# Kernel optimization log

Measured on AMD Instinct MI355X. Metric: run time of the kernel, lower is better.

The kernel has to match this reference:

```python
import jax, jax.numpy as jnp
import numpy as np

EPS = 1e-5


def _bn(x, g, b, axis):
    # training-mode BatchNorm1d (biased variance, eps=1e-5)
    m = x.mean(axis=axis, keepdims=True)
    v = x.var(axis=axis, keepdims=True)
    return (x - m) * jax.lax.rsqrt(v + EPS) * g + b


def _masked_softmax(s, mask):
    # softmax over each node's neighbor set; exact zeros elsewhere
    neg = jnp.finfo(s.dtype).min
    m = jnp.max(jnp.where(mask, s, neg), axis=-1, keepdims=True)
    p = jnp.where(mask, jnp.exp(s - m), 0.0)
    return p / p.sum(axis=-1, keepdims=True)


def _gcn_layer(xh, W, b, g, beta, Wa, ba, mask, apply_act):
    # xh: [H,N,Din] -> [H,N,Dout]; per-head Linear + BatchNorm over nodes
    h = jnp.einsum('hnd,hdo->hno', xh, W) + b[:, None, :]
    h = _bn(h, g[:, None, :], beta[:, None, :], axis=1)
    # dense GAT-style scores [H,N,N], LeakyReLU(0.2)
    s = jnp.einsum('hno,hom->hnm', h, Wa) + ba[:, None, :]
    s = jnp.where(s >= 0, s, 0.2 * s)
    # original detaches scores (numpy roundtrip) -> no grad through attention
    att = jax.lax.stop_gradient(_masked_softmax(s, mask))
    out = jnp.einsum('hnm,hmo->hno', att, h)
    return jax.nn.elu(out) if apply_act else out


def _forward(x, adj_mask, target_X, target,
             W0, b0, g0, beta0, Wa0, ba0,
             W1, b1, g1, beta1, Wa1, ba1,
             bng, bnb, Wp1, bp1, gp1, betap1, Wp2, bp2):
    H = W0.shape[0]
    xh = jnp.broadcast_to(x[None], (H,) + x.shape)            # replicate per head
    h = _gcn_layer(xh, W0, b0, g0, beta0, Wa0, ba0, adj_mask, True)
    h = _gcn_layer(h, W1, b1, g1, beta1, Wa1, ba1, adj_mask, False)
    out = h.sum(axis=0) / H                                    # head average [N,out]
    out = jax.nn.elu(_bn(out, bng, bnb, axis=0))
    y = jax.nn.elu(_bn(out @ Wp1 + bp1, gp1, betap1, axis=0))  # pred1
    y = y @ Wp2 + bp2                                          # pred2
    logits = y[target_X]                                       # [T,C]
    logp = jax.nn.log_softmax(logits, axis=-1)
    loss = -jnp.take_along_axis(logp, target[:, None], axis=-1).mean()
    return loss, logits


def setup_inputs() -> dict:
    key = jax.random.key(0)
    N, H, IN, H1, OUT, PRED, C, T, DEG = 4096, 4, 512, 256, 128, 64, 8, 512, 32
    ks = jax.random.split(key, 16)
    rng = np.random.default_rng(0)
    nbr = rng.integers(0, N, size=(N, DEG))
    mask = np.zeros((N, N), dtype=bool)
    mask[np.arange(N)[:, None], nbr] = True  # every row non-empty

    def lin(k, fan_in, shape):
        return jax.random.normal(k, shape, jnp.float32) / np.sqrt(fan_in)

    return {
        'x': jax.random.normal(ks[0], (N, IN), jnp.float32),
        'adj_mask': jnp.asarray(mask),
        'target_X': jax.random.randint(ks[1], (T,), 0, N),
        'target': jax.random.randint(ks[2], (T,), 0, C),
        'W0': lin(ks[3], IN, (H, IN, H1)), 'b0': jnp.zeros((H, H1)),
        'g0': jnp.ones((H, H1)), 'beta0': jnp.zeros((H, H1)),
        'Wa0': lin(ks[4], H1, (H, H1, N)), 'ba0': jnp.zeros((H, N)),
        'W1': lin(ks[5], H1, (H, H1, OUT)), 'b1': jnp.zeros((H, OUT)),
        'g1': jnp.ones((H, OUT)), 'beta1': jnp.zeros((H, OUT)),
        'Wa1': lin(ks[6], OUT, (H, OUT, N)), 'ba1': jnp.zeros((H, N)),
        'bng': jnp.ones((OUT,)), 'bnb': jnp.zeros((OUT,)),
        'Wp1': lin(ks[7], OUT, (OUT, PRED)), 'bp1': jnp.zeros((PRED,)),
        'gp1': jnp.ones((PRED,)), 'betap1': jnp.zeros((PRED,)),
        'Wp2': lin(ks[8], PRED, (PRED, C)), 'bp2': jnp.zeros((C,)),
    }


def reference(x, adj_mask, target_X, target,
              W0, b0, g0, beta0, Wa0, ba0,
              W1, b1, g1, beta1, Wa1, ba1,
              bng, bnb, Wp1, bp1, gp1, betap1, Wp2, bp2):
    return _forward(x, adj_mask, target_X, target,
                    W0, b0, g0, beta0, Wa0, ba0,
                    W1, b1, g1, beta1, Wa1, ba1,
                    bng, bnb, Wp1, bp1, gp1, betap1, Wp2, bp2)
```

## Files before the change

### kernel.cpp

```cpp
#include <hip/hip_runtime.h>
#include <hip/hip_bf16.h>
#include <math.h>

#define NN   4096
#define HH   4
#define DIN  512
#define DH1  256
#define DOUT 128
#define DPRED 64
#define NCLS 8
#define NT   512
#define NBMAX 32
#define BNCH 128

typedef __attribute__((ext_vector_type(4))) float f32x4;
typedef __attribute__((ext_vector_type(8))) short bf16x8;
typedef __attribute__((ext_vector_type(8))) unsigned short u16x8;

#define SWZ(o) ((o) + (((o) >> 5) << 2))

__device__ __forceinline__ float b2f(unsigned short u) {
    return __uint_as_float(((unsigned)u) << 16);
}

__device__ __forceinline__ void gload_lds16(const __hip_bfloat16* g, __hip_bfloat16* l) {
    __builtin_amdgcn_global_load_lds(
        (__attribute__((address_space(1))) void*)(g),
        (__attribute__((address_space(3))) void*)(l), 16, 0, 0);
}

#define PREP_BLOCKS 9856
__global__ __launch_bounds__(256) void prep_k(
    const void* __restrict__ mask,
    int* __restrict__ nbr_cnt, int* __restrict__ nbr_idx,
    const float* __restrict__ x, __hip_bfloat16* __restrict__ xbf,
    const float* __restrict__ W0, __hip_bfloat16* __restrict__ W0T,
    const float* __restrict__ W1, __hip_bfloat16* __restrict__ W1T,
    const float* __restrict__ Wa0, __hip_bfloat16* __restrict__ WaT0,
    const float* __restrict__ Wa1, __hip_bfloat16* __restrict__ WaT1) {
    __shared__ float tbuf[32][33];
    __shared__ int md;
    int bid = blockIdx.x, tid = threadIdx.x;

    if (bid < 1024) {
        int n0 = bid * 4;
        if (tid == 0) md = 0;
        __syncthreads();
        const uint4* mb4 = (const uint4*)((const char*)mask + (long)n0 * NN);
        unsigned acc = 0;
        for (int i = tid; i < 1024; i += 256) {
            uint4 v = mb4[i];
            acc |= (v.x | v.y | v.z | v.w);
        }
        if (acc & 0x0000FF00u) atomicOr(&md, 1);
        __syncthreads();
        int byteMode = md;
        int wave = tid >> 6, lane = tid & 63;
        int n = n0 + wave;
        long base = (long)n * NN;
        int cnt = 0;
        unsigned long long ltmask = (1ull << lane) - 1ull;
        if (byteMode) {
            const unsigned* mwb = (const unsigned*)((const char*)mask + base);
            for (int j0 = 0; j0 < NN; j0 += 256) {
                unsigned w = mwb[(j0 >> 2) + lane];
                unsigned m4 = 0;
                if (w & 0x000000FFu) m4 |= 1;
                if (w & 0x0000FF00u) m4 |= 2;
                if (w & 0x00FF0000u) m4 |= 4;
                if (w & 0xFF000000u) m4 |= 8;
                unsigned long long bal0 = __ballot(m4 & 1);
                unsigned long long bal1 = __ballot(m4 & 2);
                unsigned long long bal2 = __ballot(m4 & 4);
                unsigned long long bal3 = __ballot(m4 & 8);
                int below = __popcll(bal0 & ltmask) + __popcll(bal1 & ltmask)
                          + __popcll(bal2 & ltmask) + __popcll(bal3 & ltmask);
                int same = 0;
#pragma unroll
                for (int b = 0; b < 4; ++b) {
                    if ((m4 >> b) & 1) {
                        int pos = cnt + below + same;
                        if (pos < NBMAX) nbr_idx[n * NBMAX + pos] = j0 + lane * 4 + b;
                        ++same;
                    }
                }
                cnt += __popcll(bal0) + __popcll(bal1) + __popcll(bal2) + __popcll(bal3);
            }
        } else {
            const int* mw = (const int*)((const char*)mask + base * 4);
            for (int j0 = 0; j0 < NN; j0 += 64) {
                int j = j0 + lane;
                int nz = (mw[j] != 0);
                unsigned long long bal = __ballot(nz);
                int pre = __popcll(bal & ltmask);
                if (nz) {
                    int pos = cnt + pre;
                    if (pos < NBMAX) nbr_idx[n * NBMAX + pos] = j;
                }
                cnt += __popcll(bal);
            }
        }
        if (lane == 0) nbr_cnt[n] = cnt > NBMAX ? NBMAX : cnt;
        return;
    }

    if (bid < 3072) {
        int i = (bid - 1024) * 256 + tid;
        float4 v = ((const float4*)x)[i];
        __hip_bfloat16* o = xbf + (long)i * 4;
        o[0] = __float2bfloat16(v.x); o[1] = __float2bfloat16(v.y);
        o[2] = __float2bfloat16(v.z); o[3] = __float2bfloat16(v.w);
        return;
    }

    const float* in; __hip_bfloat16* outp; int R, Cc, cx, cy, b;
    if (bid < 3584) {
        int idx = bid - 3072; in = W0; outp = W0T; R = DIN; Cc = DH1;
        cx = idx & 7; cy = (idx >> 3) & 15; b = idx >> 7;
    } else if (bid < 3712) {
        int idx = bid - 3584; in = W1; outp = W1T; R = DH1; Cc = DOUT;
        cx = idx & 3; cy = (idx >> 2) & 7; b = idx >> 5;
    } else if (bid < 7808) {
        int idx = bid - 3712; in = Wa0; outp = WaT0; R = DH1; Cc = NN;
        cx = idx & 127; cy = (idx >> 7) & 7; b = idx >> 10;
    } else {
        int idx = bid - 7808; in = Wa1; outp = WaT1; R = DOUT; Cc = NN;
        cx = idx & 127; cy = (idx >> 7) & 3; b = idx >> 9;
    }
    {
        int xx = tid & 31, yy = tid >> 5;
        const float* ib = in + (long)b * R * Cc;
        __hip_bfloat16* ob = outp + (long)b * R * Cc;
        int c0 = cx * 32, r0 = cy * 32;
        for (int i = 0; i < 32; i += 8) tbuf[yy + i][xx] = ib[(long)(r0 + yy + i) * Cc + c0 + xx];
        __syncthreads();
        for (int i = 0; i < 32; i += 8)
            ob[(long)(c0 + yy + i) * R + r0 + xx] = __float2bfloat16(tbuf[xx][yy + i]);
    }
}

__global__ __launch_bounds__(256) void gemm_bf16_k(
    const __hip_bfloat16* __restrict__ A, long aBS,
    const __hip_bfloat16* __restrict__ BT, long bBS,
    __hip_bfloat16* __restrict__ C, int M, int N, int K) {
    __shared__ __hip_bfloat16 Al[128 * 32];
    __shared__ __hip_bfloat16 Bl[128 * 32];
    int b = blockIdx.z;
    const __hip_bfloat16* Ab = A + (long)b * aBS;
    const __hip_bfloat16* Bb = BT + (long)b * bBS;
    int m0 = blockIdx.x * 128, n0 = blockIdx.y * 128;
    int t = threadIdx.x;
    int lane = t & 63, wid = t >> 6;
    int wr = wid >> 1, wc = wid & 1;
    int lr = lane & 15, lg = lane >> 4;
    f32x4 acc[4][4] = {};
    for (int k0 = 0; k0 < K; k0 += 32) {
#pragma unroll
        for (int p = 0; p < 2; ++p) {
            int c = p * 256 + t;
            int row = c >> 2, cb = (c & 3) * 8;
            gload_lds16(Ab + (long)(m0 + row) * K + k0 + cb, &Al[(p * 256 + (t & 192)) * 8]);
            gload_lds16(Bb + (long)(n0 + row) * K + k0 + cb, &Bl[(p * 256 + (t & 192)) * 8]);
        }
        __syncthreads();
        bf16x8 af[4], bfr[4];
#pragma unroll
        for (int i = 0; i < 4; ++i)
            af[i] = *(const bf16x8*)&Al[(wr * 64 + i * 16 + lr) * 32 + lg * 8];
#pragma unroll
        for (int j = 0; j < 4; ++j)
            bfr[j] = *(const bf16x8*)&Bl[(wc * 64 + j * 16 + lr) * 32 + lg * 8];
#pragma unroll
        for (int i = 0; i < 4; ++i)
#pragma unroll
            for (int j = 0; j < 4; ++j)
                acc[i][j] = __builtin_amdgcn_mfma_f32_16x16x32_bf16(af[i], bfr[j], acc[i][j], 0, 0, 0);
        __syncthreads();
    }
#pragma unroll
    for (int i = 0; i < 4; ++i) {
#pragma unroll
        for (int j = 0; j < 4; ++j) {
            int row = m0 + wr * 64 + i * 16 + lg * 4;
            int col = n0 + wc * 64 + j * 16 + lr;
#pragma unroll
            for (int r = 0; r < 4; ++r)
                C[((long)b * M + row + r) * N + col] = __float2bfloat16(acc[i][j][r]);
        }
    }
}

__global__ void gemm_aff_f32(const float* __restrict__ A, int lda,
                             const float* __restrict__ Bw, int ldb,
                             const float* __restrict__ Aaff, const float* __restrict__ Baff,
                             float* __restrict__ C, int M, int N, int K) {
    __shared__ float As[16][64];
    __shared__ float Bs[16][68];
    int m0 = blockIdx.x * 64, n0 = blockIdx.y * 64;
    int tid = threadIdx.x;
    int tx = tid & 15, ty = tid >> 4;
    float acc[4][4] = {};
    for (int k0 = 0; k0 < K; k0 += 16) {
        {
            int r = tid >> 2, c = (tid & 3) * 4;
            float4 v = *(const float4*)(A + (long)(m0 + r) * lda + k0 + c);
            float a0 = Aaff[k0 + c + 0], b0 = Baff[k0 + c + 0];
            float a1 = Aaff[k0 + c + 1], b1 = Baff[k0 + c + 1];
            float a2 = Aaff[k0 + c + 2], b2 = Baff[k0 + c + 2];
            float a3 = Aaff[k0 + c + 3], b3 = Baff[k0 + c + 3];
            v.x = v.x * a0 + b0; v.x = v.x > 0.f ? v.x : expm1f(v.x);
            v.y = v.y * a1 + b1; v.y = v.y > 0.f ? v.y : expm1f(v.y);
            v.z = v.z * a2 + b2; v.z = v.z > 0.f ? v.z : expm1f(v.z);
            v.w = v.w * a3 + b3; v.w = v.w > 0.f ? v.w : expm1f(v.w);
            As[c + 0][r] = v.x; As[c + 1][r] = v.y; As[c + 2][r] = v.z; As[c + 3][r] = v.w;
        }
        {
            int r = tid >> 4, c = (tid & 15) * 4;
            float4 v = *(const float4*)(Bw + (long)(k0 + r) * ldb + n0 + c);
            *(float4*)&Bs[r][c] = v;
        }
        __syncthreads();
#pragma unroll
        for (int kk = 0; kk < 16; ++kk) {
            float a[4], bb[4];
#pragma unroll
            for (int i = 0; i < 4; ++i) a[i] = As[kk][ty * 4 + i];
#pragma unroll
            for (int j = 0; j < 4; ++j) bb[j] = Bs[kk][tx * 4 + j];
#pragma unroll
            for (int i = 0; i < 4; ++i)
#pragma unroll
                for (int j = 0; j < 4; ++j)
                    acc[i][j] += a[i] * bb[j];
        }
        __syncthreads();
    }
#pragma unroll
    for (int i = 0; i < 4; ++i) {
        int m = m0 + ty * 4 + i;
#pragma unroll
        for (int j = 0; j < 4; ++j)
            C[((long)m) * N + n0 + tx * 4 + j] = acc[i][j];
    }
}

template <int D, int CH>
__global__ void bn_part_bf_k(const __hip_bfloat16* __restrict__ x, int Mrows,
                             float* __restrict__ ps, float* __restrict__ ps2) {
    int c = blockIdx.x, b = blockIdx.y;
    int o = threadIdx.x;
    int rows = Mrows / CH;
    const unsigned short* xb = (const unsigned short*)(x + (long)b * Mrows * D);
    float s = 0.f, s2 = 0.f;
    for (int r = 0; r < rows; ++r) {
        float v = b2f(xb[(long)(c * rows + r) * D + o]);
        s += v; s2 += v * v;
    }
    ps[((b * CH) + c) * D + o] = s;
    ps2[((b * CH) + c) * D + o] = s2;
}

template <int D, int CH>
__global__ void bn_part_k(const float* __restrict__ x, int Mrows,
                          float* __restrict__ ps, float* __restrict__ ps2) {
    int c = blockIdx.x, b = blockIdx.y;
    int o = threadIdx.x;
    int rows = Mrows / CH;
    const float* xb = x + (long)b * Mrows * D;
    float s = 0.f, s2 = 0.f;
    for (int r = 0; r < rows; ++r) {
        float v = xb[(long)(c * rows + r) * D + o];
        s += v; s2 += v * v;
    }
    ps[((b * CH) + c) * D + o] = s;
    ps2[((b * CH) + c) * D + o] = s2;
}

__global__ void avgbn_k(const float* __restrict__ l1, float* __restrict__ avg,
                        float* __restrict__ ps, float* __restrict__ ps2) {
    int c = blockIdx.x;
    int o = threadIdx.x;
    const long S = (long)NN * DOUT;
    int rows = NN / BNCH;
    float s = 0.f, s2 = 0.f;
    for (int r = 0; r < rows; ++r) {
        long i = (long)(c * rows + r) * DOUT + o;
        float v = 0.25f * (l1[i] + l1[i + S] + l1[i + 2 * S] + l1[i + 3 * S]);
        avg[i] = v;
        s += v; s2 += v * v;
    }
    ps[c * DOUT + o] = s;
    ps2[c * DOUT + o] = s2;
}

template <int D, int CH>
__global__ void bn_fin_k(const float* __restrict__ ps, const float* __restrict__ ps2,
                         int Mrows, const float* __restrict__ g, const float* __restrict__ beta,
                         float* __restrict__ Aarr, float* __restrict__ Barr) {
    int b = blockIdx.x, o = threadIdx.x;
    float s = 0.f, s2 = 0.f;
    for (int c = 0; c < CH; ++c) {
        s += ps[((b * CH) + c) * D + o];
        s2 += ps2[((b * CH) + c) * D + o];
    }
    float mean = s / Mrows;
    float var = s2 / Mrows - mean * mean;
    float inv = 1.0f / sqrtf(var + 1e-5f);
    float Ag = g[b * D + o] * inv;
    Aarr[b * D + o] = Ag;
    Barr[b * D + o] = beta[b * D + o] - mean * Ag;
}

template <int D, int OUTBF>
__global__ __launch_bounds__(D) void attn9_k(
    const __hip_bfloat16* __restrict__ h,
    const __hip_bfloat16* __restrict__ WaT,
    const float* __restrict__ ba,
    const int* __restrict__ nbr_cnt, const int* __restrict__ nbr_idx,
    const float* __restrict__ Aarr, const float* __restrict__ Barr,
    void* __restrict__ outv, int applyElu) {
    constexpr int NW = D / 64;
    constexpr int NG = D / 16;
    constexpr int EPG = D / 16;
    constexpr int E = D / 64;
    constexpr int KPW = NBMAX / NW;
    using u16xE = __attribute__((ext_vector_type(E))) unsigned short;

    __shared__ float hrowF[D + (D >> 5) * 4];
    __shared__ float sc[NBMAX];
    __shared__ int nb[NBMAX];
    __shared__ float part[NW][D];
    __shared__ int scnt;
    int n = blockIdx.x, hd = blockIdx.y;
    int tid = threadIdx.x;
    const unsigned short* hbu = (const unsigned short*)(h + (long)hd * NN * D);
    const unsigned short* wbu = (const unsigned short*)(WaT + (long)hd * NN * D);
    hrowF[SWZ(tid)] = b2f(hbu[(long)n * D + tid]) * Aarr[hd * D + tid] + Barr[hd * D + tid];
    if (tid == 0) scnt = nbr_cnt[n];
    if (tid < NBMAX) nb[tid] = nbr_idx[n * NBMAX + tid];
    __syncthreads();
    int cnt = scnt;
    int wv = tid >> 6, ln = tid & 63;

    u16xE pre[KPW];
#pragma unroll
    for (int i = 0; i < KPW; ++i) {
        int kk = wv * KPW + i;
        if (kk < cnt) pre[i] = *(const u16xE*)(hbu + (long)nb[kk] * D + ln * E);
    }

    int g = tid >> 4, j = tid & 15;
    for (int k = g; k < cnt; k += NG) {
        int m = nb[k];
        const unsigned short* wr = wbu + (long)m * D + j * EPG;
        float acc = 0.f;
#pragma unroll
        for (int c = 0; c < EPG / 8; ++c) {
            u16x8 v = *(const u16x8*)(wr + c * 8);
            const float* hp = &hrowF[SWZ(j * EPG + c * 8)];
#pragma unroll
            for (int e = 0; e < 8; ++e)
                acc += hp[e] * b2f(v[e]);
        }
#pragma unroll
        for (int s = 8; s; s >>= 1) acc += __shfl_xor(acc, s);
        if (j == 0) {
            float sv = acc + ba[(long)hd * NN + m];
            sc[k] = sv >= 0.f ? sv : 0.2f * sv;
        }
    }
    __syncthreads();

    if (tid < 64) {
        float s = (tid < cnt) ? sc[tid] : -INFINITY;
        float mx = s;
#pragma unroll
        for (int t = 32; t; t >>= 1) mx = fmaxf(mx, __shfl_xor(mx, t));
        float p = (tid < cnt) ? expf(s - mx) : 0.f;
        float sum = p;
#pragma unroll
        for (int t = 32; t; t >>= 1) sum += __shfl_xor(sum, t);
        if (tid < cnt) sc[tid] = p / sum;
    }
    __syncthreads();

    float acc[E] = {};
#pragma unroll
    for (int i = 0; i < KPW; ++i) {
        int kk = wv * KPW + i;
        if (kk < cnt) {
            float w = sc[kk];
#pragma unroll
            for (int e = 0; e < E; ++e) acc[e] += w * b2f(pre[i][e]);
        }
    }
#pragma unroll
    for (int e = 0; e < E; ++e) part[wv][ln * E + e] = acc[e];
    __syncthreads();
    float v = 0.f;
#pragma unroll
    for (int w2 = 0; w2 < NW; ++w2) v += part[w2][tid];
    v = v * Aarr[hd * D + tid] + Barr[hd * D + tid];
    if (applyElu) v = v > 0.f ? v : expm1f(v);
    long oidx = ((long)hd * NN + n) * D + tid;
    if (OUTBF) ((__hip_bfloat16*)outv)[oidx] = __float2bfloat16(v);
    else ((float*)outv)[oidx] = v;
}

__global__ __launch_bounds__(512) void pred2loss_k(
    const float* __restrict__ p1, const int* __restrict__ tX, const int* __restrict__ tgt,
    const float* __restrict__ Ap, const float* __restrict__ Bp,
    const float* __restrict__ Wp2, const float* __restrict__ bp2,
    float* __restrict__ out) {
    __shared__ float red[512];
    int t = threadIdx.x;
    const float* row = p1 + (long)tX[t] * DPRED;
    float v[DPRED];
#pragma unroll
    for (int j = 0; j < DPRED; ++j) {
        float u = row[j] * Ap[j] + Bp[j];
        v[j] = u > 0.f ? u : expm1f(u);
    }
    float lg[NCLS];
#pragma unroll
    for (int c = 0; c < NCLS; ++c) {
        float a = bp2[c];
        for (int j = 0; j < DPRED; ++j) a += v[j] * Wp2[j * NCLS + c];
        lg[c] = a;
        out[1 + t * NCLS + c] = a;
    }
    float mx = lg[0];
#pragma unroll
    for (int c = 1; c < NCLS; ++c) mx = fmaxf(mx, lg[c]);
    float se = 0.f;
#pragma unroll
    for (int c = 0; c < NCLS; ++c) se += expf(lg[c] - mx);
    float lse = mx + logf(se);
    int tg = tgt[t];
    float lt = lg[0];
#pragma unroll
    for (int c = 1; c < NCLS; ++c) lt = (c == tg) ? lg[c] : lt;
    red[t] = lse - lt;
    __syncthreads();
    for (int s = 256; s; s >>= 1) {
        if (t < s) red[t] += red[t + s];
        __syncthreads();
    }
    if (t == 0) out[0] = red[0] / (float)NT;
}

extern "C" void kernel_launch(void* const* d_in, const int* in_sizes, int n_in,
                              void* d_out, int out_size, void* d_ws, size_t ws_size,
                              hipStream_t stream) {
    const float* x     = (const float*)d_in[0];
    const void*  adj   = d_in[1];
    const int*   tX    = (const int*)d_in[2];
    const int*   tgt   = (const int*)d_in[3];
    const float* W0    = (const float*)d_in[4];
    const float* g0    = (const float*)d_in[6];
    const float* beta0 = (const float*)d_in[7];
    const float* Wa0   = (const float*)d_in[8];
    const float* ba0   = (const float*)d_in[9];
    const float* W1    = (const float*)d_in[10];
    const float* g1    = (const float*)d_in[12];
    const float* beta1 = (const float*)d_in[13];
    const float* Wa1   = (const float*)d_in[14];
    const float* ba1   = (const float*)d_in[15];
    const float* bng   = (const float*)d_in[16];
    const float* bnb   = (const float*)d_in[17];
    const float* Wp1   = (const float*)d_in[18];
    const float* gp1   = (const float*)d_in[20];
    const float* betap1= (const float*)d_in[21];
    const float* Wp2   = (const float*)d_in[22];
    const float* bp2   = (const float*)d_in[23];
    float* out = (float*)d_out;

    char* ws = (char*)d_ws;
    size_t off = 0;
    auto alloc = [&](size_t b) { size_t o = off; off = (off + b + 255) & ~(size_t)255; return o; };
    int*   nbr_cnt = (int*)(ws + alloc(NN * 4));
    int*   nbr_idx = (int*)(ws + alloc((size_t)NN * NBMAX * 4));
    float* ps      = (float*)(ws + alloc((size_t)HH * BNCH * DH1 * 4));
    float* ps2     = (float*)(ws + alloc((size_t)HH * BNCH * DH1 * 4));
    float* Aarr    = (float*)(ws + alloc((size_t)HH * DH1 * 4));
    float* Barr    = (float*)(ws + alloc((size_t)HH * DH1 * 4));
    __hip_bfloat16* xbf   = (__hip_bfloat16*)(ws + alloc((size_t)NN * DIN * 2));
    __hip_bfloat16* W0T   = (__hip_bfloat16*)(ws + alloc((size_t)HH * DH1 * DIN * 2));
    __hip_bfloat16* W1T   = (__hip_bfloat16*)(ws + alloc((size_t)HH * DOUT * DH1 * 2));
    __hip_bfloat16* WaT0b = (__hip_bfloat16*)(ws + alloc((size_t)HH * NN * DH1 * 2));
    __hip_bfloat16* WaT1b = (__hip_bfloat16*)(ws + alloc((size_t)HH * NN * DOUT * 2));
    __hip_bfloat16* h0bf  = (__hip_bfloat16*)(ws + alloc((size_t)HH * NN * DH1 * 2));
    __hip_bfloat16* g1bf  = (__hip_bfloat16*)(ws + alloc((size_t)HH * NN * DH1 * 2));
    __hip_bfloat16* h1bf  = (__hip_bfloat16*)(ws + alloc((size_t)HH * NN * DOUT * 2));
    float* l1out = (float*)(ws + alloc((size_t)HH * NN * DOUT * 4));
    float* avg   = (float*)(ws + alloc((size_t)NN * DOUT * 4));
    float* p1    = (float*)(ws + alloc((size_t)NN * DPRED * 4));

    prep_k<<<PREP_BLOCKS, 256, 0, stream>>>(adj, nbr_cnt, nbr_idx, x, xbf,
                                            W0, W0T, W1, W1T, Wa0, WaT0b, Wa1, WaT1b);

    gemm_bf16_k<<<dim3(NN / 128, DH1 / 128, HH), 256, 0, stream>>>(
        xbf, 0L, W0T, (long)DH1 * DIN, h0bf, NN, DH1, DIN);
    bn_part_bf_k<DH1, BNCH><<<dim3(BNCH, HH), DH1, 0, stream>>>(h0bf, NN, ps, ps2);
    bn_fin_k<DH1, BNCH><<<HH, DH1, 0, stream>>>(ps, ps2, NN, g0, beta0, Aarr, Barr);
    attn9_k<DH1, 1><<<dim3(NN, HH), DH1, 0, stream>>>(
        h0bf, WaT0b, ba0, nbr_cnt, nbr_idx, Aarr, Barr, g1bf, 1);

    gemm_bf16_k<<<dim3(NN / 128, 1, HH), 256, 0, stream>>>(
        g1bf, (long)NN * DH1, W1T, (long)DOUT * DH1, h1bf, NN, DOUT, DH1);
    bn_part_bf_k<DOUT, BNCH><<<dim3(BNCH, HH), DOUT, 0, stream>>>(h1bf, NN, ps, ps2);
    bn_fin_k<DOUT, BNCH><<<HH, DOUT, 0, stream>>>(ps, ps2, NN, g1, beta1, Aarr, Barr);
    attn9_k<DOUT, 0><<<dim3(NN, HH), DOUT, 0, stream>>>(
        h1bf, WaT1b, ba1, nbr_cnt, nbr_idx, Aarr, Barr, l1out, 0);

    avgbn_k<<<BNCH, DOUT, 0, stream>>>(l1out, avg, ps, ps2);
    bn_fin_k<DOUT, BNCH><<<1, DOUT, 0, stream>>>(ps, ps2, NN, bng, bnb, Aarr, Barr);

    gemm_aff_f32<<<dim3(NN / 64, 1, 1), 256, 0, stream>>>(
        avg, DOUT, Wp1, DPRED, Aarr, Barr, p1, NN, DPRED, DOUT);
    bn_part_k<DPRED, BNCH><<<dim3(BNCH, 1), DPRED, 0, stream>>>(p1, NN, ps, ps2);
    bn_fin_k<DPRED, BNCH><<<1, DPRED, 0, stream>>>(ps, ps2, NN, gp1, betap1, Aarr, Barr);

    pred2loss_k<<<1, 512, 0, stream>>>(p1, tX, tgt, Aarr, Barr, Wp2, bp2, out);
}
```

Baseline: 242.9 us.

## Use bf16 dot2 for attention scores and 256-thread blocks for both layers

The attention kernel now stores the normalized query row as packed bf16 pairs in shared memory and computes neighbor scores with the bf16 fdot2 intrinsic instead of scalar fp32 multiply-adds. The layer-2 attention (D=128) is launched with 256 threads, so 16 groups score neighbors and 4 waves split the aggregation, giving more parallelism per node. The goal is to halve the arithmetic and LDS traffic in the score loop. The trade-off is that rounding the BN-normalized query to bf16 adds precision loss to the scores, and half the threads sit idle in some phases when D=128.

```diff
diff --git a/kernel.cpp b/kernel.cpp
--- a/kernel.cpp
+++ b/kernel.cpp
@@ -17,10 +17,35 @@
 typedef __attribute__((ext_vector_type(8))) short bf16x8;
 typedef __attribute__((ext_vector_type(8))) unsigned short u16x8;
 
-#define SWZ(o) ((o) + (((o) >> 5) << 2))
+#if defined(__has_builtin)
+#if __has_builtin(__builtin_amdgcn_fdot2_f32_bf16)
+#define HAVE_DOT2 1
+typedef __attribute__((ext_vector_type(2))) __bf16 bf16x2_t;
+#endif
+#endif
+
+#define SWZP(o) ((o) + ((o) >> 4))
 
 __device__ __forceinline__ float b2f(unsigned short u) {
     return __uint_as_float(((unsigned)u) << 16);
+}
+__device__ __forceinline__ unsigned short f2b(float f) {
+    __hip_bfloat16 h = __float2bfloat16(f);
+    return *(unsigned short*)&h;
+}
+
+__device__ __forceinline__ float pair_dot(unsigned wpair, unsigned qpair, float acc) {
+#ifdef HAVE_DOT2
+    union { unsigned u; bf16x2_t v; } w, q;
+    w.u = wpair; q.u = qpair;
+    return __builtin_amdgcn_fdot2_f32_bf16(w.v, q.v, acc, false);
+#else
+    float wl = __uint_as_float(wpair << 16);
+    float wh = __uint_as_float(wpair & 0xFFFF0000u);
+    float ql = __uint_as_float(qpair << 16);
+    float qh = __uint_as_float(qpair & 0xFFFF0000u);
+    return acc + wl * ql + wh * qh;
+#endif
 }
 
 __device__ __forceinline__ void gload_lds16(const __hip_bfloat16* g, __hip_bfloat16* l) {
@@ -312,21 +337,22 @@
 }
 
 template <int D, int OUTBF>
-__global__ __launch_bounds__(D) void attn9_k(
+__global__ __launch_bounds__(256) void attn10_k(
     const __hip_bfloat16* __restrict__ h,
     const __hip_bfloat16* __restrict__ WaT,
     const float* __restrict__ ba,
     const int* __restrict__ nbr_cnt, const int* __restrict__ nbr_idx,
     const float* __restrict__ Aarr, const float* __restrict__ Barr,
     void* __restrict__ outv, int applyElu) {
-    constexpr int NW = D / 64;
-    constexpr int NG = D / 16;
+    constexpr int NW = 4;
+    constexpr int NG = 16;
     constexpr int EPG = D / 16;
+    constexpr int PPL = EPG / 2;
     constexpr int E = D / 64;
     constexpr int KPW = NBMAX / NW;
     using u16xE = __attribute__((ext_vector_type(E))) unsigned short;
 
-    __shared__ float hrowF[D + (D >> 5) * 4];
+    __shared__ unsigned qp[D / 2 + D / 32 + 1];
     __shared__ float sc[NBMAX];
     __shared__ int nb[NBMAX];
     __shared__ float part[NW][D];
@@ -335,7 +361,14 @@
     int tid = threadIdx.x;
     const unsigned short* hbu = (const unsigned short*)(h + (long)hd * NN * D);
     const unsigned short* wbu = (const unsigned short*)(WaT + (long)hd * NN * D);
-    hrowF[SWZ(tid)] = b2f(hbu[(long)n * D + tid]) * Aarr[hd * D + tid] + Barr[hd * D + tid];
+    if (tid < D / 2) {
+        unsigned hp = *(const unsigned*)(hbu + (long)n * D + tid * 2);
+        float2 av = *(const float2*)(Aarr + hd * D + tid * 2);
+        float2 bv = *(const float2*)(Barr + hd * D + tid * 2);
+        float lo = b2f((unsigned short)(hp & 0xFFFFu)) * av.x + bv.x;
+        float hi = b2f((unsigned short)(hp >> 16)) * av.y + bv.y;
+        qp[SWZP(tid)] = (unsigned)f2b(lo) | ((unsigned)f2b(hi) << 16);
+    }
     if (tid == 0) scnt = nbr_cnt[n];
     if (tid < NBMAX) nb[tid] = nbr_idx[n * NBMAX + tid];
     __syncthreads();
@@ -350,18 +383,15 @@
     }
 
     int g = tid >> 4, j = tid & 15;
-    for (int k = g; k < cnt; k += NG) {
+#pragma unroll
+    for (int k = g; k < NBMAX; k += NG) {
+        if (k >= cnt) break;
         int m = nb[k];
-        const unsigned short* wr = wbu + (long)m * D + j * EPG;
+        const unsigned* wrp = (const unsigned*)(wbu + (long)m * D) + j * PPL;
         float acc = 0.f;
 #pragma unroll
-        for (int c = 0; c < EPG / 8; ++c) {
-            u16x8 v = *(const u16x8*)(wr + c * 8);
-            const float* hp = &hrowF[SWZ(j * EPG + c * 8)];
-#pragma unroll
-            for (int e = 0; e < 8; ++e)
-                acc += hp[e] * b2f(v[e]);
-        }
+        for (int c = 0; c < PPL; ++c)
+            acc = pair_dot(wrp[c], qp[SWZP(j * PPL + c)], acc);
 #pragma unroll
         for (int s = 8; s; s >>= 1) acc += __shfl_xor(acc, s);
         if (j == 0) {
@@ -397,14 +427,14 @@
 #pragma unroll
     for (int e = 0; e < E; ++e) part[wv][ln * E + e] = acc[e];
     __syncthreads();
-    float v = 0.f;
-#pragma unroll
-    for (int w2 = 0; w2 < NW; ++w2) v += part[w2][tid];
-    v = v * Aarr[hd * D + tid] + Barr[hd * D + tid];
-    if (applyElu) v = v > 0.f ? v : expm1f(v);
-    long oidx = ((long)hd * NN + n) * D + tid;
-    if (OUTBF) ((__hip_bfloat16*)outv)[oidx] = __float2bfloat16(v);
-    else ((float*)outv)[oidx] = v;
+    if (tid < D) {
+        float v = part[0][tid] + part[1][tid] + part[2][tid] + part[3][tid];
+        v = v * Aarr[hd * D + tid] + Barr[hd * D + tid];
+        if (applyElu) v = v > 0.f ? v : expm1f(v);
+        long oidx = ((long)hd * NN + n) * D + tid;
+        if (OUTBF) ((__hip_bfloat16*)outv)[oidx] = __float2bfloat16(v);
+        else ((float*)outv)[oidx] = v;
+    }
 }
 
 __global__ __launch_bounds__(512) void pred2loss_k(
@@ -503,14 +533,14 @@
         xbf, 0L, W0T, (long)DH1 * DIN, h0bf, NN, DH1, DIN);
     bn_part_bf_k<DH1, BNCH><<<dim3(BNCH, HH), DH1, 0, stream>>>(h0bf, NN, ps, ps2);
     bn_fin_k<DH1, BNCH><<<HH, DH1, 0, stream>>>(ps, ps2, NN, g0, beta0, Aarr, Barr);
-    attn9_k<DH1, 1><<<dim3(NN, HH), DH1, 0, stream>>>(
+    attn10_k<DH1, 1><<<dim3(NN, HH), 256, 0, stream>>>(
         h0bf, WaT0b, ba0, nbr_cnt, nbr_idx, Aarr, Barr, g1bf, 1);
 
     gemm_bf16_k<<<dim3(NN / 128, 1, HH), 256, 0, stream>>>(
         g1bf, (long)NN * DH1, W1T, (long)DOUT * DH1, h1bf, NN, DOUT, DH1);
     bn_part_bf_k<DOUT, BNCH><<<dim3(BNCH, HH), DOUT, 0, stream>>>(h1bf, NN, ps, ps2);
     bn_fin_k<DOUT, BNCH><<<HH, DOUT, 0, stream>>>(ps, ps2, NN, g1, beta1, Aarr, Barr);
-    attn9_k<DOUT, 0><<<dim3(NN, HH), DOUT, 0, stream>>>(
+    attn10_k<DOUT, 0><<<dim3(NN, HH), 256, 0, stream>>>(
         h1bf, WaT1b, ba1, nbr_cnt, nbr_idx, Aarr, Barr, l1out, 0);
 
     avgbn_k<<<BNCH, DOUT, 0, stream>>>(l1out, avg, ps, ps2);
```

After: 244.2 us. No clear change (+0.5%).
